# Performance work log

Hardware: AMD Instinct MI355X
Metric: run time of the kernel (lower is better)

The kernel has to match this reference:

```python
import jax, jax.numpy as jnp
import numpy as np

N_NODES = 50000      # nodes per side (12500 tetrahedra x 4 nodes)
N_GRAPHS = 12500     # graph pairs in the batch
HID = 256


def _tet_edges(n_graphs):
    # 12 directed edges among the 4 nodes of each tetrahedron
    pat = np.array([(a, b) for a in range(4) for b in range(4) if a != b], dtype=np.int64)  # [12,2]
    base = np.arange(n_graphs, dtype=np.int64)[:, None, None] * 4  # [G,1,1]
    ei = (base + pat[None]).reshape(-1, 2).T  # [2, 12*G]
    return jnp.asarray(ei)


def setup_inputs() -> dict:
    key = jax.random.key(0)
    ks = jax.random.split(key, 20)

    def w(k, shape, fan_in):
        return (jax.random.normal(k, shape, dtype=jnp.float32) / np.sqrt(fan_in)).astype(jnp.float32)

    x_1 = jax.random.normal(ks[0], (N_NODES, 3), dtype=jnp.float32)
    x_2 = jax.random.normal(ks[1], (N_NODES, 3), dtype=jnp.float32)
    edge_index_1 = _tet_edges(N_GRAPHS)
    edge_index_2 = _tet_edges(N_GRAPHS)
    batch_1 = jnp.repeat(jnp.arange(N_GRAPHS, dtype=jnp.int64), 4)
    batch_2 = batch_1

    params = dict(
        W1=w(ks[2], (3, HID), 3), b1=jnp.zeros((HID,), jnp.float32),
        W2=w(ks[3], (HID, HID), HID), b2=jnp.zeros((HID,), jnp.float32),
        W3=w(ks[4], (HID, HID), HID), b3=jnp.zeros((HID,), jnp.float32),
        Wl1=w(ks[5], (512, 512), 512), bl1=jnp.zeros((512,), jnp.float32),
        Wl2=w(ks[6], (512, 256), 512), bl2=jnp.zeros((256,), jnp.float32),
        Wl3=w(ks[7], (256, 128), 256), bl3=jnp.zeros((128,), jnp.float32),
        Wl4=w(ks[8], (128, 64), 128), bl4=jnp.zeros((64,), jnp.float32),
    )
    return dict(x_1=x_1, edge_index_1=edge_index_1, batch_1=batch_1,
                x_2=x_2, edge_index_2=edge_index_2, batch_2=batch_2, **params)


def gcn_conv(x, edge_index, W, b):
    # PyG GCNConv: add self loops, symmetric deg normalization, sum aggregate, then bias
    n = x.shape[0]
    loops = jnp.arange(n, dtype=edge_index.dtype)
    src = jnp.concatenate([edge_index[0], loops])
    dst = jnp.concatenate([edge_index[1], loops])
    deg = jax.ops.segment_sum(jnp.ones_like(dst, dtype=x.dtype), dst, num_segments=n)
    dis = jnp.where(deg > 0, jax.lax.rsqrt(jnp.maximum(deg, 1.0)), 0.0)
    norm = dis[src] * dis[dst]                       # [E+N]
    xw = x @ W                                       # [N, out]
    out = jax.ops.segment_sum(norm[:, None] * xw[src], dst, num_segments=n)
    return out + b


def encode(x, edge_index, batch, W1, b1, W2, b2, W3, b3):
    x = jax.nn.relu(gcn_conv(x, edge_index, W1, b1))
    x = jax.nn.relu(gcn_conv(x, edge_index, W2, b2))
    x = jax.nn.relu(gcn_conv(x, edge_index, W3, b3))
    # global_mean_pool
    s = jax.ops.segment_sum(x, batch, num_segments=N_GRAPHS)
    cnt = jax.ops.segment_sum(jnp.ones((x.shape[0],), x.dtype), batch, num_segments=N_GRAPHS)
    return s / jnp.maximum(cnt, 1.0)[:, None]


def reference(x_1, edge_index_1, batch_1, x_2, edge_index_2, batch_2,
              W1, b1, W2, b2, W3, b3,
              Wl1, bl1, Wl2, bl2, Wl3, bl3, Wl4, bl4):
    h1 = encode(x_1, edge_index_1, batch_1, W1, b1, W2, b2, W3, b3)
    h2 = encode(x_2, edge_index_2, batch_2, W1, b1, W2, b2, W3, b3)
    h = jnp.concatenate([h1, h2], axis=1)            # [G, 512]
    h = jax.nn.relu(h @ Wl1 + bl1)
    h = jax.nn.relu(h @ Wl2 + bl2)
    h = jax.nn.relu(h @ Wl3 + bl3)
    h = h @ Wl4 + bl4                                # layer_4: no relu (as in source)
    return jax.nn.sigmoid(h)                         # [G, 64]
```

## Files before the change

kernel.cpp:

```cpp
#include <hip/hip_runtime.h>


typedef _Float16 half8 __attribute__((ext_vector_type(8)));
typedef float floatx4 __attribute__((ext_vector_type(4)));

struct PrepArgsV13 { const float* in[6]; };

__global__ __launch_bounds__(256) void v13_prep(PrepArgsV13 p, _Float16* Bf) {
  const int frags[6] = {8192, 8192, 32768, 16384, 4096, 1024};
  const int lgN[6]   = {8, 8, 9, 8, 7, 6};
  const int off[6]   = {0, 65536, 131072, 393216, 524288, 557056};
  int f = blockIdx.x * 256 + threadIdx.x;
  for (int i = 0; i < 6; ++i) {
    if (f < frags[i]) {
      int N = 1 << lgN[i];
      int lane = f & 63, rem = f >> 6;
      int nt = rem & ((N >> 4) - 1);
      int kb = rem >> (lgN[i] - 4);
      int n = nt * 16 + (lane & 15);
      int k0 = kb * 32 + (lane >> 4) * 8;
      const float* src = p.in[i] + (size_t)k0 * N + n;
      half8 v;
#pragma unroll
      for (int j = 0; j < 8; ++j) v[j] = (_Float16)src[(size_t)j * N];
      *(half8*)(Bf + off[i] + (size_t)f * 8) = v;
      return;
    }
    f -= frags[i];
  }
}

template<int MT, int NT, int TNT, int KB, bool ENC_IN, int OUT_MODE>
__device__ __forceinline__ void layer(
    const _Float16* __restrict__ Bf, const float* __restrict__ bias,
    _Float16* sA, float* __restrict__ outg, int pair0, int nw, int m0, int lane) {
  const int quad = lane >> 4, lr = lane & 15;
  const int n0 = nw * (NT * 16);
  const int STRIDE = ENC_IN ? 264 : 520;
  const _Float16* bp = Bf + ((size_t)(nw * NT) * 64 + lane) * 8;

  floatx4 acc[MT][NT];
#pragma unroll
  for (int mt = 0; mt < MT; ++mt)
#pragma unroll
    for (int nt = 0; nt < NT; ++nt)
      acc[mt][nt] = (floatx4){0.f, 0.f, 0.f, 0.f};

  half8 bbuf[3][NT];
#pragma unroll
  for (int nt = 0; nt < NT; ++nt) {
    bbuf[0][nt] = *(const half8*)(bp + nt * 512);
    bbuf[1][nt] = *(const half8*)(bp + (size_t)TNT * 512 + nt * 512);
  }

#pragma unroll
  for (int kb = 0; kb < KB; ++kb) {
    const int cur = kb % 3;
    half8 av[MT];
#pragma unroll
    for (int mt = 0; mt < MT; ++mt)
      av[mt] = *(const half8*)(sA + (m0 + mt * 16 + lr) * STRIDE + kb * 32 + quad * 8);
#pragma unroll
    for (int nt = 0; nt < NT; ++nt)
#pragma unroll
      for (int mt = 0; mt < MT; ++mt)
        acc[mt][nt] = __builtin_amdgcn_mfma_f32_16x16x32_f16(av[mt], bbuf[cur][nt], acc[mt][nt], 0, 0, 0);
    if (kb + 2 < KB) {
      const int nxt = (kb + 2) % 3;
#pragma unroll
      for (int nt = 0; nt < NT; ++nt)
        bbuf[nxt][nt] = *(const half8*)(bp + (size_t)(kb + 2) * (TNT * 512) + nt * 512);
    }
  }

  __syncthreads();

#pragma unroll
  for (int nt = 0; nt < NT; ++nt) {
    int c = n0 + nt * 16 + lr;
    float bv = bias[c];
#pragma unroll
    for (int mt = 0; mt < MT; ++mt) {
#pragma unroll
      for (int reg = 0; reg < 4; ++reg) {
        int r = m0 + mt * 16 + quad * 4 + reg;
        float v = acc[mt][nt][reg] + bv;
        if (OUT_MODE <= 2) {
          v = fmaxf(v, 0.f);
          int a;
          if (OUT_MODE == 0)      a = r * 264 + c;
          else if (OUT_MODE == 1) a = (r >> 1) * 520 + (r & 1) * 256 + c;
          else                    a = r * 520 + c;
          sA[a] = (_Float16)v;
        } else {
          if (r < 50) outg[(size_t)(pair0 + r) * 64 + c] = 1.0f / (1.0f + expf(-v));
        }
      }
    }
  }
  __syncthreads();
}

__global__ __launch_bounds__(1024) void v13_mega(
    const float* __restrict__ x1, const float* __restrict__ x2,
    const float* __restrict__ W1, const float* __restrict__ b1,
    const _Float16* __restrict__ Bf,
    const float* __restrict__ b2, const float* __restrict__ b3,
    const float* __restrict__ bl1, const float* __restrict__ bl2,
    const float* __restrict__ bl3, const float* __restrict__ bl4,
    float* __restrict__ outg) {
  __shared__ _Float16 sA[33280];
  __shared__ float sM[112][3];

  int tid = threadIdx.x;
  int wave = tid >> 6, lane = tid & 63;
  int pair0 = blockIdx.x * 50;

  for (int i = tid; i < 16640; i += 1024) ((float*)sA)[i] = 0.f;

  if (tid < 112) {
    int r = tid;
    float a0 = 0.f, a1 = 0.f, a2 = 0.f;
    if (r < 100) {
      int g = pair0 + (r >> 1);
      const float* q = ((r & 1) ? x2 : x1) + (size_t)g * 12;
      a0 = 0.25f * (q[0] + q[3] + q[6] + q[9]);
      a1 = 0.25f * (q[1] + q[4] + q[7] + q[10]);
      a2 = 0.25f * (q[2] + q[5] + q[8] + q[11]);
    }
    sM[r][0] = a0; sM[r][1] = a1; sM[r][2] = a2;
  }
  __syncthreads();

  {
    int c = tid & 255;
    float w0 = W1[c], w1 = W1[256 + c], w2 = W1[512 + c], bb = b1[c];
    for (int r = (tid >> 8); r < 112; r += 4) {
      float v = fmaxf(sM[r][0] * w0 + sM[r][1] * w1 + sM[r][2] * w2 + bb, 0.f);
      sA[r * 264 + c] = (_Float16)v;
    }
  }
  __syncthreads();

  layer<7, 1, 16,  8, true,  0>(Bf + 0,      b2,  sA, nullptr, pair0, wave, 0, lane);
  layer<7, 1, 16,  8, true,  1>(Bf + 65536,  b3,  sA, nullptr, pair0, wave, 0, lane);
  layer<4, 2, 32, 16, false, 2>(Bf + 131072, bl1, sA, nullptr, pair0, wave, 0, lane);
  layer<4, 1, 16, 16, false, 2>(Bf + 393216, bl2, sA, nullptr, pair0, wave, 0, lane);
  layer<2, 1,  8,  8, false, 2>(Bf + 524288, bl3, sA, nullptr, pair0,
                                wave & 7, (wave >> 3) * 32, lane);
  layer<1, 1,  4,  4, false, 3>(Bf + 557056, bl4, sA, outg,    pair0,
                                wave & 3, (wave >> 2) * 16, lane);
}

extern "C" void kernel_launch(void* const* d_in, const int* in_sizes, int n_in,
                              void* d_out, int out_size, void* d_ws, size_t ws_size,
                              hipStream_t stream) {
  const float* x1  = (const float*)d_in[0];
  const float* x2  = (const float*)d_in[3];
  const float* W1  = (const float*)d_in[6];
  const float* b1  = (const float*)d_in[7];
  const float* W2  = (const float*)d_in[8];
  const float* b2  = (const float*)d_in[9];
  const float* W3  = (const float*)d_in[10];
  const float* b3  = (const float*)d_in[11];
  const float* Wl1 = (const float*)d_in[12];
  const float* bl1 = (const float*)d_in[13];
  const float* Wl2 = (const float*)d_in[14];
  const float* bl2 = (const float*)d_in[15];
  const float* Wl3 = (const float*)d_in[16];
  const float* bl3 = (const float*)d_in[17];
  const float* Wl4 = (const float*)d_in[18];
  const float* bl4 = (const float*)d_in[19];

  _Float16* Bf = (_Float16*)d_ws;

  PrepArgsV13 pa;
  pa.in[0] = W2;  pa.in[1] = W3;  pa.in[2] = Wl1;
  pa.in[3] = Wl2; pa.in[4] = Wl3; pa.in[5] = Wl4;

  v13_prep<<<dim3(276), dim3(256), 0, stream>>>(pa, Bf);
  v13_mega<<<dim3(250), dim3(1024), 0, stream>>>(x1, x2, W1, b1, Bf,
                                                 b2, b3, bl1, bl2, bl3, bl4,
                                                 (float*)d_out);
}
```

Baseline: 121.7 us.

## Ping-pong LDS activation buffers and halve block size with wider per-wave tiles

Activations now alternate between two shared-memory buffers, so each layer reads one and writes the other. This removes the barrier between a layer's MFMA loop and its epilogue writes. The block shrinks from 1024 to 512 threads, and each wave covers twice as many N tiles (more accumulators per wave), with launch bounds asking for two blocks per CU. LDS use doubles to about 133 KB per block, so two blocks per CU may not fit, and the extra accumulator registers could cut occupancy. Only the padding rows of the first buffer are zeroed now.

After: 124.1 us. About the same (+2.0%).

```diff
diff --git a/kernel.cpp b/kernel.cpp
--- a/kernel.cpp
+++ b/kernel.cpp
@@ -4,9 +4,9 @@
 typedef _Float16 half8 __attribute__((ext_vector_type(8)));
 typedef float floatx4 __attribute__((ext_vector_type(4)));
 
-struct PrepArgsV13 { const float* in[6]; };
+struct PrepArgsV14 { const float* in[6]; };
 
-__global__ __launch_bounds__(256) void v13_prep(PrepArgsV13 p, _Float16* Bf) {
+__global__ __launch_bounds__(256) void v14_prep(PrepArgsV14 p, _Float16* Bf) {
   const int frags[6] = {8192, 8192, 32768, 16384, 4096, 1024};
   const int lgN[6]   = {8, 8, 9, 8, 7, 6};
   const int off[6]   = {0, 65536, 131072, 393216, 524288, 557056};
@@ -33,7 +33,8 @@
 template<int MT, int NT, int TNT, int KB, bool ENC_IN, int OUT_MODE>
 __device__ __forceinline__ void layer(
     const _Float16* __restrict__ Bf, const float* __restrict__ bias,
-    _Float16* sA, float* __restrict__ outg, int pair0, int nw, int m0, int lane) {
+    const _Float16* __restrict__ srcA, _Float16* dstA, float* __restrict__ outg,
+    int pair0, int nw, int m0, int lane) {
   const int quad = lane >> 4, lr = lane & 15;
   const int n0 = nw * (NT * 16);
   const int STRIDE = ENC_IN ? 264 : 520;
@@ -59,7 +60,7 @@
     half8 av[MT];
 #pragma unroll
     for (int mt = 0; mt < MT; ++mt)
-      av[mt] = *(const half8*)(sA + (m0 + mt * 16 + lr) * STRIDE + kb * 32 + quad * 8);
+      av[mt] = *(const half8*)(srcA + (m0 + mt * 16 + lr) * STRIDE + kb * 32 + quad * 8);
 #pragma unroll
     for (int nt = 0; nt < NT; ++nt)
 #pragma unroll
@@ -72,8 +73,6 @@
         bbuf[nxt][nt] = *(const half8*)(bp + (size_t)(kb + 2) * (TNT * 512) + nt * 512);
     }
   }
-
-  __syncthreads();
 
 #pragma unroll
   for (int nt = 0; nt < NT; ++nt) {
@@ -91,7 +90,7 @@
           if (OUT_MODE == 0)      a = r * 264 + c;
           else if (OUT_MODE == 1) a = (r >> 1) * 520 + (r & 1) * 256 + c;
           else                    a = r * 520 + c;
-          sA[a] = (_Float16)v;
+          dstA[a] = (_Float16)v;
         } else {
           if (r < 50) outg[(size_t)(pair0 + r) * 64 + c] = 1.0f / (1.0f + expf(-v));
         }
@@ -101,7 +100,7 @@
   __syncthreads();
 }
 
-__global__ __launch_bounds__(1024) void v13_mega(
+__global__ __launch_bounds__(512, 2) void v14_mega(
     const float* __restrict__ x1, const float* __restrict__ x2,
     const float* __restrict__ W1, const float* __restrict__ b1,
     const _Float16* __restrict__ Bf,
@@ -109,14 +108,15 @@
     const float* __restrict__ bl1, const float* __restrict__ bl2,
     const float* __restrict__ bl3, const float* __restrict__ bl4,
     float* __restrict__ outg) {
-  __shared__ _Float16 sA[33280];
+  __shared__ _Float16 sB0[33280];
+  __shared__ _Float16 sB1[33280];
   __shared__ float sM[112][3];
 
   int tid = threadIdx.x;
   int wave = tid >> 6, lane = tid & 63;
   int pair0 = blockIdx.x * 50;
 
-  for (int i = tid; i < 16640; i += 1024) ((float*)sA)[i] = 0.f;
+  for (int i = tid; i < 2080; i += 512) ((float*)sB0)[14560 + i] = 0.f;
 
   if (tid < 112) {
     int r = tid;
@@ -135,21 +135,20 @@
   {
     int c = tid & 255;
     float w0 = W1[c], w1 = W1[256 + c], w2 = W1[512 + c], bb = b1[c];
-    for (int r = (tid >> 8); r < 112; r += 4) {
+    for (int r = (tid >> 8); r < 112; r += 2) {
       float v = fmaxf(sM[r][0] * w0 + sM[r][1] * w1 + sM[r][2] * w2 + bb, 0.f);
-      sA[r * 264 + c] = (_Float16)v;
+      sB0[r * 264 + c] = (_Float16)v;
     }
   }
   __syncthreads();
 
-  layer<7, 1, 16,  8, true,  0>(Bf + 0,      b2,  sA, nullptr, pair0, wave, 0, lane);
-  layer<7, 1, 16,  8, true,  1>(Bf + 65536,  b3,  sA, nullptr, pair0, wave, 0, lane);
-  layer<4, 2, 32, 16, false, 2>(Bf + 131072, bl1, sA, nullptr, pair0, wave, 0, lane);
-  layer<4, 1, 16, 16, false, 2>(Bf + 393216, bl2, sA, nullptr, pair0, wave, 0, lane);
-  layer<2, 1,  8,  8, false, 2>(Bf + 524288, bl3, sA, nullptr, pair0,
-                                wave & 7, (wave >> 3) * 32, lane);
-  layer<1, 1,  4,  4, false, 3>(Bf + 557056, bl4, sA, outg,    pair0,
-                                wave & 3, (wave >> 2) * 16, lane);
+  layer<7, 2, 16,  8, true,  0>(Bf + 0,      b2,  sB0, sB1, nullptr, pair0, wave, 0, lane);
+  layer<7, 2, 16,  8, true,  1>(Bf + 65536,  b3,  sB1, sB0, nullptr, pair0, wave, 0, lane);
+  layer<4, 4, 32, 16, false, 2>(Bf + 131072, bl1, sB0, sB1, nullptr, pair0, wave, 0, lane);
+  layer<4, 2, 16, 16, false, 2>(Bf + 393216, bl2, sB1, sB0, nullptr, pair0, wave, 0, lane);
+  layer<4, 1,  8,  8, false, 2>(Bf + 524288, bl3, sB0, sB1, nullptr, pair0, wave, 0, lane);
+  layer<2, 1,  4,  4, false, 3>(Bf + 557056, bl4, sB1, nullptr, outg, pair0,
+                                wave & 3, (wave >> 2) * 32, lane);
 }
 
 extern "C" void kernel_launch(void* const* d_in, const int* in_sizes, int n_in,
@@ -174,12 +173,12 @@
 
   _Float16* Bf = (_Float16*)d_ws;
 
-  PrepArgsV13 pa;
+  PrepArgsV14 pa;
   pa.in[0] = W2;  pa.in[1] = W3;  pa.in[2] = Wl1;
   pa.in[3] = Wl2; pa.in[4] = Wl3; pa.in[5] = Wl4;
 
-  v13_prep<<<dim3(276), dim3(256), 0, stream>>>(pa, Bf);
-  v13_mega<<<dim3(250), dim3(1024), 0, stream>>>(x1, x2, W1, b1, Bf,
-                                                 b2, b3, bl1, bl2, bl3, bl4,
-                                                 (float*)d_out);
+  v14_prep<<<dim3(276), dim3(256), 0, stream>>>(pa, Bf);
+  v14_mega<<<dim3(250), dim3(512), 0, stream>>>(x1, x2, W1, b1, Bf,
+                                                b2, b3, bl1, bl2, bl3, bl4,
+                                                (float*)d_out);
 }
```
